# Optimization experiments

Measured on AMD Instinct MI355X. Metric: run time of the kernel, lower is better.

The kernel has to match this reference:

```python
import jax, jax.numpy as jnp
import numpy as np

HEADS = 8
EPS = 1e-5

def setup_inputs() -> dict:
    key = jax.random.key(0)
    k1, k2, k3 = jax.random.split(key, 3)
    b, c, n = 4, 512, 2048
    x = jax.random.normal(k1, (b, c, n), dtype=jnp.float32)
    g = jnp.ones((c,), dtype=jnp.float32)
    w_qkv = jax.random.normal(k2, (3 * c, c), dtype=jnp.float32) * (1.0 / np.sqrt(c))
    w_out = jax.random.normal(k3, (c, c), dtype=jnp.float32) * (1.0 / np.sqrt(c))
    b_out = jnp.zeros((c,), dtype=jnp.float32)
    return {"x": x, "g": g, "w_qkv": w_qkv, "w_out": w_out, "b_out": b_out}

def reference(x, g, w_qkv, w_out, b_out):
    b, c, n = x.shape
    h = HEADS
    d = c // h
    scale = d ** -0.5
    # channel LayerNorm (biased variance), scale g, no bias
    mean = jnp.mean(x, axis=1, keepdims=True)
    var = jnp.var(x, axis=1, keepdims=True)
    xn = (x - mean) * jax.lax.rsqrt(var + EPS) * g[None, :, None]
    # 1x1 conv == channel matmul: (3c, c) x (b, c, n) -> (b, 3c, n)
    qkv = jnp.einsum('oc,bcn->bon', w_qkv, xn)
    q, k, v = jnp.split(qkv, 3, axis=1)
    # b (h d) n -> b h d n
    q = q.reshape(b, h, d, n) * scale
    k = k.reshape(b, h, d, n)
    v = v.reshape(b, h, d, n)
    sim = jnp.einsum('bhdi,bhdj->bhij', q, k)  # [b,h,n,n]
    attn = jax.nn.softmax(sim, axis=-1)
    out = jnp.einsum('bhij,bhdj->bhid', attn, v)  # [b,h,n,d]
    out = out.transpose(0, 1, 3, 2).reshape(b, h * d, n)  # b (h d) n
    out = jnp.einsum('oc,bcn->bon', w_out, out) + b_out[None, :, None]
    return out
```

## Files before the change

### kernel.cpp

```cpp
#include <hip/hip_runtime.h>
#include <hip/hip_bf16.h>

#define B_ 4
#define C_ 512
#define N_ 2048
#define H_ 8
#define D_ 64
#define O3_ 1536
#define SPLIT 2
#define JTN 16

typedef __bf16 bf16x8 __attribute__((ext_vector_type(8)));
typedef float f32x4 __attribute__((ext_vector_type(4)));
typedef unsigned short ushort_t;

#define QSCALE 0.1803368801111137f

__device__ inline ushort_t f2b(float f) {
    __hip_bfloat16 h = __float2bfloat16(f);
    return *reinterpret_cast<ushort_t*>(&h);
}
__device__ inline float b2f(ushort_t u) {
    unsigned v = ((unsigned)u) << 16;
    return *reinterpret_cast<float*>(&v);
}

__device__ inline void gload16(const ushort_t* g, ushort_t* l) {
    __builtin_amdgcn_global_load_lds(
        (const __attribute__((address_space(1))) unsigned int*)g,
        (__attribute__((address_space(3))) unsigned int*)l, 16, 0, 0);
}

__global__ __launch_bounds__(256) void k_pre(const float* __restrict__ x,
                                             const float* __restrict__ g,
                                             ushort_t* __restrict__ xnT,
                                             const float* __restrict__ wqkv,
                                             const float* __restrict__ wout,
                                             ushort_t* __restrict__ wqkv_b,
                                             ushort_t* __restrict__ wout_b) {
    if (blockIdx.x >= 256) {
        int i = (blockIdx.x - 256) * 256 + threadIdx.x;
        float4 a = reinterpret_cast<const float4*>(wqkv)[i];
        ushort4 o;
        o.x = f2b(a.x); o.y = f2b(a.y); o.z = f2b(a.z); o.w = f2b(a.w);
        reinterpret_cast<ushort4*>(wqkv_b)[i] = o;
        if (i < 65536) {
            float4 c = reinterpret_cast<const float4*>(wout)[i];
            ushort4 oc;
            oc.x = f2b(c.x); oc.y = f2b(c.y); oc.z = f2b(c.z); oc.w = f2b(c.w);
            reinterpret_cast<ushort4*>(wout_b)[i] = oc;
        }
        return;
    }

    int bid = blockIdx.x;
    int b  = bid >> 6;
    int j0 = (bid & 63) * 32;
    int t  = threadIdx.x;

    __shared__ float s_red[8][32];
    __shared__ float s_red2[8][32];
    __shared__ float s_mean[32], s_rstd[32];
    __shared__ float s_g[C_];
    __shared__ __align__(16) ushort_t s_t[32][C_ + 2];

    for (int i = t; i < C_; i += 256) s_g[i] = g[i];

    int jl = t & 31, cg = t >> 5;
    const float* xb = x + (size_t)b * C_ * N_;

    float xv[64];
    float sum = 0.f, sq = 0.f;
#pragma unroll
    for (int i = 0; i < 64; ++i) {
        float v = xb[(size_t)(cg * 64 + i) * N_ + j0 + jl];
        xv[i] = v;
        sum += v; sq += v * v;
    }
    s_red[cg][jl] = sum; s_red2[cg][jl] = sq;
    __syncthreads();
    if (t < 32) {
        float s = 0.f, q = 0.f;
#pragma unroll
        for (int i = 0; i < 8; ++i) { s += s_red[i][t]; q += s_red2[i][t]; }
        float mean = s * (1.0f / C_);
        float var  = q * (1.0f / C_) - mean * mean;
        s_mean[t] = mean;
        s_rstd[t] = rsqrtf(var + 1e-5f);
    }
    __syncthreads();

    float mean = s_mean[jl], rstd = s_rstd[jl];
#pragma unroll
    for (int i = 0; i < 64; ++i) {
        int c = cg * 64 + i;
        s_t[jl][c] = f2b((xv[i] - mean) * rstd * s_g[c]);
    }
    __syncthreads();

    for (int jr = 0; jr < 32; ++jr) {
        unsigned val = *reinterpret_cast<const unsigned*>(&s_t[jr][t * 2]);
        *reinterpret_cast<unsigned*>(
            &xnT[((size_t)(b * N_ + j0 + jr)) * C_ + t * 2]) = val;
    }
}

template <int MODE>
__global__ __launch_bounds__(256) void k_gemm(const ushort_t* __restrict__ A,
                                              const ushort_t* __restrict__ Bt,
                                              ushort_t* __restrict__ qT,
                                              ushort_t* __restrict__ kT,
                                              ushort_t* __restrict__ vv,
                                              float* __restrict__ out,
                                              const float* __restrict__ b_out) {
    constexpr int M = (MODE == 0) ? O3_ : C_;
    constexpr int K = C_;
    constexpr int NMT = M / 128;
    constexpr int NWG = B_ * NMT * 16;

    int bid  = blockIdx.x;
    int sbid = (bid & 7) * (NWG / 8) + (bid >> 3);
    int b    = sbid / (NMT * 16);
    int rem  = sbid % (NMT * 16);
    int mt0  = (rem / 16) * 128;
    int nt0  = (rem % 16) * 128;

    int t = threadIdx.x;
    int w = t >> 6, lane = t & 63;
    int wm = (w >> 1) * 64, wn = (w & 1) * 64;
    int low = lane & 15, hi = lane >> 4;

    __shared__ __align__(16) ushort_t sA[128][64];
    __shared__ __align__(16) ushort_t sB[128][64];

    const ushort_t* Bb = Bt + (size_t)b * N_ * K;

    int srow = lane >> 3;
    int sseg = (lane & 7) ^ srow;
    const ushort_t* Ag = A  + (size_t)(mt0 + w * 32 + srow) * K + sseg * 8;
    const ushort_t* Bg = Bb + (size_t)(nt0 + w * 32 + srow) * K + sseg * 8;

    f32x4 acc[4][4] = {};

    for (int k0 = 0; k0 < K; k0 += 64) {
#pragma unroll
        for (int i = 0; i < 4; ++i) {
            gload16(Ag + (size_t)(i * 8) * K + k0, &sA[w * 32 + i * 8][0]);
            gload16(Bg + (size_t)(i * 8) * K + k0, &sB[w * 32 + i * 8][0]);
        }
        asm volatile("s_waitcnt vmcnt(0)" ::: "memory");
        __syncthreads();
#pragma unroll
        for (int kk = 0; kk < 64; kk += 32) {
            bf16x8 af[4], bfr[4];
#pragma unroll
            for (int mt = 0; mt < 4; ++mt) {
                int cseg = ((kk >> 3) + hi) ^ (low & 7);
                af[mt] = *reinterpret_cast<const bf16x8*>(
                    &sA[wm + mt * 16 + low][cseg * 8]);
            }
#pragma unroll
            for (int nt = 0; nt < 4; ++nt) {
                int cseg = ((kk >> 3) + hi) ^ (low & 7);
                bfr[nt] = *reinterpret_cast<const bf16x8*>(
                    &sB[wn + nt * 16 + low][cseg * 8]);
            }
#pragma unroll
            for (int mt = 0; mt < 4; ++mt)
#pragma unroll
                for (int nt = 0; nt < 4; ++nt)
                    acc[mt][nt] = __builtin_amdgcn_mfma_f32_16x16x32_bf16(
                        af[mt], bfr[nt], acc[mt][nt], 0, 0, 0);
        }
        __syncthreads();
    }

#pragma unroll
    for (int mt = 0; mt < 4; ++mt)
#pragma unroll
        for (int nt = 0; nt < 4; ++nt) {
            int m0 = mt0 + wm + mt * 16 + hi * 4;
            int j  = nt0 + wn + nt * 16 + low;
            if constexpr (MODE == 0) {
                if (m0 < 512) {
                    ushort4 pk;
                    pk.x = f2b(acc[mt][nt][0] * QSCALE);
                    pk.y = f2b(acc[mt][nt][1] * QSCALE);
                    pk.z = f2b(acc[mt][nt][2] * QSCALE);
                    pk.w = f2b(acc[mt][nt][3] * QSCALE);
                    *reinterpret_cast<ushort4*>(
                        &qT[(((size_t)(b * H_ + (m0 >> 6)) * N_) + j) * D_ +
                            (m0 & 63)]) = pk;
                } else if (m0 < 1024) {
                    int mm = m0 - 512;
                    ushort4 pk;
                    pk.x = f2b(acc[mt][nt][0]);
                    pk.y = f2b(acc[mt][nt][1]);
                    pk.z = f2b(acc[mt][nt][2]);
                    pk.w = f2b(acc[mt][nt][3]);
                    *reinterpret_cast<ushort4*>(
                        &kT[(((size_t)(b * H_ + (mm >> 6)) * N_) + j) * D_ +
                            (mm & 63)]) = pk;
                } else {
                    int mm0 = m0 - 1024;
#pragma unroll
                    for (int r = 0; r < 4; ++r)
                        vv[(((size_t)(b * H_ + (mm0 >> 6)) * D_) +
                            ((mm0 & 63) + r)) * N_ + j] = f2b(acc[mt][nt][r]);
                }
            } else {
#pragma unroll
                for (int r = 0; r < 4; ++r)
                    out[((size_t)(b * C_ + m0 + r)) * N_ + j] =
                        acc[mt][nt][r] + b_out[m0 + r];
            }
        }
}

__global__ __launch_bounds__(512, 4) void k_attn(const ushort_t* __restrict__ qT,
                                                 const ushort_t* __restrict__ kT,
                                                 const ushort_t* __restrict__ vv,
                                                 ushort_t* __restrict__ O0,
                                                 ushort_t* __restrict__ O1,
                                                 float* __restrict__ Lp) {
    int bid  = blockIdx.x;
    int sbid = ((bid & 7) << 6) | (bid >> 3);
    int it256 = sbid & 7;
    int s     = (sbid >> 3) & 1;
    int h     = (sbid >> 4) & 7;
    int b     = sbid >> 7;
    int i0    = it256 * 256;
    int t = threadIdx.x, w = t >> 6, lane = t & 63;
    int low = lane & 15, hi = lane >> 4;

    __shared__ ushort_t sK[2][64][64];
    __shared__ ushort_t sV[2][64][64];
    __shared__ __align__(16) ushort_t sPT[256][72];

    const ushort_t* qb = qT + ((size_t)(b * H_ + h)) * N_ * D_;
    const ushort_t* kb = kT + ((size_t)(b * H_ + h)) * N_ * D_;
    const ushort_t* vb = vv + ((size_t)(b * H_ + h)) * D_ * N_;

    int srow = lane >> 3;
    int sseg = (lane & 7) ^ srow;
    const ushort_t* kg = kb + (size_t)(w * 8 + srow) * D_ + sseg * 8;
    const ushort_t* vg = vb + (size_t)(w * 8 + srow) * N_ + sseg * 8;

    bf16x8 qf[2][2];
#pragma unroll
    for (int mt = 0; mt < 2; ++mt)
#pragma unroll
        for (int kx = 0; kx < 2; ++kx)
            qf[mt][kx] = *reinterpret_cast<const bf16x8*>(
                &qb[(size_t)(i0 + w * 32 + mt * 16 + low) * D_ + kx * 32 + hi * 8]);

    {
        int j0 = s * JTN * 64;
        gload16(kg + (size_t)j0 * D_, &sK[0][w * 8][0]);
        gload16(vg + j0,              &sV[0][w * 8][0]);
    }
    asm volatile("s_waitcnt vmcnt(0)" ::: "memory");
    __syncthreads();

    f32x4 oacc[2][4] = {};
    float lp0 = 0.f, lp1 = 0.f;
    int sw = (low & 7) * 8;

    int buf = 0;
    for (int jj = 0; jj < JTN; ++jj) {
        int j0c = (s * JTN + jj) * 64;

        if (jj + 1 < JTN) {
            int j0n = j0c + 64;
            gload16(kg + (size_t)j0n * D_, &sK[buf ^ 1][w * 8][0]);
            gload16(vg + j0n,              &sV[buf ^ 1][w * 8][0]);
        }

        f32x4 sacc[2][4] = {};
#pragma unroll
        for (int kx = 0; kx < 2; ++kx) {
            bf16x8 kfx[4];
#pragma unroll
            for (int nt = 0; nt < 4; ++nt)
                kfx[nt] = *reinterpret_cast<const bf16x8*>(
                    &sK[buf][nt * 16 + low][((kx * 4 + hi) * 8) ^ sw]);
#pragma unroll
            for (int mt = 0; mt < 2; ++mt)
#pragma unroll
                for (int nt = 0; nt < 4; ++nt)
                    sacc[mt][nt] = __builtin_amdgcn_mfma_f32_16x16x32_bf16(
                        kfx[nt], qf[mt][kx], sacc[mt][nt], 0, 0, 0);
        }

        bf16x8 vf[2][4];
#pragma unroll
        for (int kx = 0; kx < 2; ++kx)
#pragma unroll
            for (int dt = 0; dt < 4; ++dt)
                vf[kx][dt] = *reinterpret_cast<const bf16x8*>(
                    &sV[buf][dt * 16 + low][((kx * 4 + hi) * 8) ^ sw]);

#pragma unroll
        for (int mt = 0; mt < 2; ++mt) {
            int qrow = w * 32 + mt * 16 + low;
#pragma unroll
            for (int nt = 0; nt < 4; ++nt) {
                float p0 = __builtin_amdgcn_exp2f(sacc[mt][nt][0]);
                float p1 = __builtin_amdgcn_exp2f(sacc[mt][nt][1]);
                float p2 = __builtin_amdgcn_exp2f(sacc[mt][nt][2]);
                float p3 = __builtin_amdgcn_exp2f(sacc[mt][nt][3]);
                if (mt == 0) lp0 += (p0 + p1) + (p2 + p3);
                else         lp1 += (p0 + p1) + (p2 + p3);
                ushort4 pk;
                pk.x = f2b(p0); pk.y = f2b(p1); pk.z = f2b(p2); pk.w = f2b(p3);
                *reinterpret_cast<ushort4*>(&sPT[qrow][nt * 16 + hi * 4]) = pk;
            }
        }

#pragma unroll
        for (int kx = 0; kx < 2; ++kx) {
            bf16x8 ap0 = *reinterpret_cast<const bf16x8*>(
                &sPT[w * 32 + low][kx * 32 + hi * 8]);
            bf16x8 ap1 = *reinterpret_cast<const bf16x8*>(
                &sPT[w * 32 + 16 + low][kx * 32 + hi * 8]);
#pragma unroll
            for (int dt = 0; dt < 4; ++dt) {
                oacc[0][dt] = __builtin_amdgcn_mfma_f32_16x16x32_bf16(
                    ap0, vf[kx][dt], oacc[0][dt], 0, 0, 0);
                oacc[1][dt] = __builtin_amdgcn_mfma_f32_16x16x32_bf16(
                    ap1, vf[kx][dt], oacc[1][dt], 0, 0, 0);
            }
        }

        asm volatile("s_waitcnt vmcnt(0)" ::: "memory");
        __syncthreads();
        buf ^= 1;
    }

    lp0 += __shfl_xor(lp0, 16); lp0 += __shfl_xor(lp0, 32);
    lp1 += __shfl_xor(lp1, 16); lp1 += __shfl_xor(lp1, 32);

    float* lrow = Lp + ((size_t)((s * B_ + b) * H_ + h)) * N_ + i0 + w * 32;
    if (lane < 16) {
        lrow[low]      = lp0;
        lrow[16 + low] = lp1;
    }

    ushort_t* op = (s == 0 ? O0 : O1) +
                   ((size_t)(b * N_ + i0 + w * 32)) * C_ + h * D_;
#pragma unroll
    for (int mt = 0; mt < 2; ++mt)
#pragma unroll
        for (int dt = 0; dt < 4; ++dt)
#pragma unroll
            for (int r = 0; r < 4; ++r)
                op[(size_t)(mt * 16 + hi * 4 + r) * C_ + dt * 16 + low] =
                    f2b(oacc[mt][dt][r]);
}

__global__ __launch_bounds__(256) void k_comb(const ushort_t* __restrict__ O1,
                                              const float* __restrict__ Lp,
                                              ushort_t* __restrict__ attnT) {
    int tid = blockIdx.x * 256 + threadIdx.x;
    int d4 = (tid & 15) * 4;
    int i  = (tid >> 4) & (N_ - 1);
    int bh = tid >> 15;
    int b = bh >> 3, h = bh & 7;
    size_t idx = ((size_t)(b * N_ + i)) * C_ + h * D_ + d4;
    ushort4 a0 = *reinterpret_cast<const ushort4*>(&attnT[idx]);
    ushort4 a1 = *reinterpret_cast<const ushort4*>(&O1[idx]);
    float l = Lp[(size_t)bh * N_ + i] + Lp[(size_t)(B_ * H_ + bh) * N_ + i];
    float linv = 1.0f / l;
    ushort4 o;
    o.x = f2b((b2f(a0.x) + b2f(a1.x)) * linv);
    o.y = f2b((b2f(a0.y) + b2f(a1.y)) * linv);
    o.z = f2b((b2f(a0.z) + b2f(a1.z)) * linv);
    o.w = f2b((b2f(a0.w) + b2f(a1.w)) * linv);
    *reinterpret_cast<ushort4*>(&attnT[idx]) = o;
}

extern "C" void kernel_launch(void* const* d_in, const int* in_sizes, int n_in,
                              void* d_out, int out_size, void* d_ws, size_t ws_size,
                              hipStream_t stream) {
    const float* x    = (const float*)d_in[0];
    const float* g    = (const float*)d_in[1];
    const float* wqkv = (const float*)d_in[2];
    const float* wout = (const float*)d_in[3];
    const float* bout = (const float*)d_in[4];
    float* out = (float*)d_out;

    char* ws = (char*)d_ws;
    ushort_t* xnT    = (ushort_t*)(ws);
    ushort_t* qT     = (ushort_t*)(ws + (size_t)8  * 1024 * 1024);
    ushort_t* kT     = (ushort_t*)(ws + (size_t)16 * 1024 * 1024);
    ushort_t* vv     = (ushort_t*)(ws + (size_t)24 * 1024 * 1024);
    ushort_t* attnT  = (ushort_t*)(ws + (size_t)32 * 1024 * 1024);
    ushort_t* wqkv_b = (ushort_t*)(ws + (size_t)40 * 1024 * 1024);
    ushort_t* wout_b = (ushort_t*)(ws + (size_t)42 * 1024 * 1024);
    float*    Lp     = (float*)   (ws + (size_t)43 * 1024 * 1024);

    k_pre<<<dim3(1024), dim3(256), 0, stream>>>(
        x, g, xnT, wqkv, wout, wqkv_b, wout_b);
    k_gemm<0><<<dim3(B_ * (O3_ / 128) * (N_ / 128)), dim3(256), 0, stream>>>(
        wqkv_b, xnT, qT, kT, vv, nullptr, nullptr);
    k_attn<<<dim3(B_ * H_ * (N_ / 256) * SPLIT), dim3(512), 0, stream>>>(
        qT, kT, vv, attnT, xnT, Lp);
    k_comb<<<dim3(4096), dim3(256), 0, stream>>>(xnT, Lp, attnT);
    k_gemm<1><<<dim3(B_ * (C_ / 128) * (N_ / 128)), dim3(256), 0, stream>>>(
        wout_b, attnT, nullptr, nullptr, nullptr, out, bout);
}
```

Before: 92.67 us.

## Add four-way KV-split attention kernel with register permlane P transpose

Adds an alternative attention kernel that splits the key/value sequence four ways instead of two. It uses 256-thread blocks in which each wave covers 64 query rows, so each K/V tile loaded into shared memory is reused across more MFMAs. The softmax probabilities are packed to bf16 and rearranged into MFMA operand layout in registers with v_permlane32/16 swap instructions. A matching combine kernel sums four partial outputs and row sums. The new path is only taken when the workspace holds the extra partial buffers, and the extra split adds more partial-output write and reduction traffic.

```diff
diff --git a/kernel.cpp b/kernel.cpp
--- a/kernel.cpp
+++ b/kernel.cpp
@@ -23,6 +23,15 @@
 __device__ inline float b2f(ushort_t u) {
     unsigned v = ((unsigned)u) << 16;
     return *reinterpret_cast<float*>(&v);
+}
+__device__ inline unsigned pkbf(float a, float b) {
+    return (unsigned)f2b(a) | ((unsigned)f2b(b) << 16);
+}
+__device__ inline void pl32swap(unsigned& a, unsigned& b) {
+    asm volatile("v_permlane32_swap_b32 %0, %1" : "+v"(a), "+v"(b));
+}
+__device__ inline void pl16swap(unsigned& a, unsigned& b) {
+    asm volatile("v_permlane16_swap_b32 %0, %1" : "+v"(a), "+v"(b));
 }
 
 __device__ inline void gload16(const ushort_t* g, ushort_t* l) {
@@ -217,6 +226,154 @@
         }
 }
 
+__global__ __launch_bounds__(256, 2) void k_attn4(const ushort_t* __restrict__ qT,
+                                                  const ushort_t* __restrict__ kT,
+                                                  const ushort_t* __restrict__ vv,
+                                                  ushort_t* __restrict__ O0,
+                                                  ushort_t* __restrict__ O1,
+                                                  ushort_t* __restrict__ O2,
+                                                  ushort_t* __restrict__ O3,
+                                                  float* __restrict__ Lp) {
+    constexpr int JT4 = 8;
+    int bid  = blockIdx.x;
+    int sbid = (bid & 7) * 128 + (bid >> 3);
+    int it256 = sbid & 7;
+    int s     = (sbid >> 3) & 3;
+    int h     = (sbid >> 5) & 7;
+    int b     = sbid >> 8;
+    int i0    = it256 * 256;
+    int t = threadIdx.x, w = t >> 6, lane = t & 63;
+    int low = lane & 15, hi = lane >> 4;
+
+    __shared__ ushort_t sK[2][64][64];
+    __shared__ ushort_t sV[2][64][64];
+
+    const ushort_t* qb = qT + ((size_t)(b * H_ + h)) * N_ * D_;
+    const ushort_t* kb = kT + ((size_t)(b * H_ + h)) * N_ * D_;
+    const ushort_t* vb = vv + ((size_t)(b * H_ + h)) * D_ * N_;
+
+    int srow = lane >> 3;
+    int sseg = (lane & 7) ^ srow;
+    const ushort_t* kg = kb + (size_t)(w * 16 + srow) * D_ + sseg * 8;
+    const ushort_t* vg = vb + (size_t)(w * 16 + srow) * N_ + sseg * 8;
+
+    bf16x8 qf[4][2];
+#pragma unroll
+    for (int mt = 0; mt < 4; ++mt)
+#pragma unroll
+        for (int kx = 0; kx < 2; ++kx)
+            qf[mt][kx] = *reinterpret_cast<const bf16x8*>(
+                &qb[(size_t)(i0 + w * 64 + mt * 16 + low) * D_ + kx * 32 + hi * 8]);
+
+    {
+        int j0 = s * JT4 * 64;
+        gload16(kg + (size_t)j0 * D_,           &sK[0][w * 16][0]);
+        gload16(kg + (size_t)(j0 + 8) * D_,     &sK[0][w * 16 + 8][0]);
+        gload16(vg + j0,                        &sV[0][w * 16][0]);
+        gload16(vg + (size_t)8 * N_ + j0,       &sV[0][w * 16 + 8][0]);
+    }
+    asm volatile("s_waitcnt vmcnt(0)" ::: "memory");
+    __syncthreads();
+
+    f32x4 oacc[4][4] = {};
+    float lp[4] = {};
+    int sw = (low & 7) * 8;
+
+    int buf = 0;
+    for (int jj = 0; jj < JT4; ++jj) {
+        if (jj + 1 < JT4) {
+            int j0n = (s * JT4 + jj + 1) * 64;
+            gload16(kg + (size_t)j0n * D_,       &sK[buf ^ 1][w * 16][0]);
+            gload16(kg + (size_t)(j0n + 8) * D_, &sK[buf ^ 1][w * 16 + 8][0]);
+            gload16(vg + j0n,                    &sV[buf ^ 1][w * 16][0]);
+            gload16(vg + (size_t)8 * N_ + j0n,   &sV[buf ^ 1][w * 16 + 8][0]);
+        }
+
+        f32x4 sacc[4][4] = {};
+#pragma unroll
+        for (int kx = 0; kx < 2; ++kx) {
+            bf16x8 kfx[4];
+#pragma unroll
+            for (int nt = 0; nt < 4; ++nt)
+                kfx[nt] = *reinterpret_cast<const bf16x8*>(
+                    &sK[buf][nt * 16 + low][((kx * 4 + hi) * 8) ^ sw]);
+#pragma unroll
+            for (int mt = 0; mt < 4; ++mt)
+#pragma unroll
+                for (int nt = 0; nt < 4; ++nt)
+                    sacc[mt][nt] = __builtin_amdgcn_mfma_f32_16x16x32_bf16(
+                        kfx[nt], qf[mt][kx], sacc[mt][nt], 0, 0, 0);
+        }
+
+        bf16x8 vf[2][4];
+#pragma unroll
+        for (int kx = 0; kx < 2; ++kx)
+#pragma unroll
+            for (int dt = 0; dt < 4; ++dt)
+                vf[kx][dt] = *reinterpret_cast<const bf16x8*>(
+                    &sV[buf][dt * 16 + low][((kx * 4 + hi) * 8) ^ sw]);
+
+#pragma unroll
+        for (int mt = 0; mt < 4; ++mt) {
+            float p[4][4];
+#pragma unroll
+            for (int nt = 0; nt < 4; ++nt)
+#pragma unroll
+                for (int r = 0; r < 4; ++r) {
+                    p[nt][r] = __builtin_amdgcn_exp2f(sacc[mt][nt][r]);
+                    lp[mt] += p[nt][r];
+                }
+#pragma unroll
+            for (int kx = 0; kx < 2; ++kx) {
+                unsigned a0 = pkbf(p[2 * kx][0],     p[2 * kx][1]);
+                unsigned a1 = pkbf(p[2 * kx][2],     p[2 * kx][3]);
+                unsigned b0 = pkbf(p[2 * kx + 1][0], p[2 * kx + 1][1]);
+                unsigned b1 = pkbf(p[2 * kx + 1][2], p[2 * kx + 1][3]);
+                pl32swap(a0, b0);
+                pl16swap(a0, b0);
+                pl32swap(a1, b1);
+                pl16swap(a1, b1);
+                unsigned tw[4] = {a0, a1, b0, b1};
+                bf16x8 pb = *reinterpret_cast<const bf16x8*>(tw);
+#pragma unroll
+                for (int dt = 0; dt < 4; ++dt)
+                    oacc[mt][dt] = __builtin_amdgcn_mfma_f32_16x16x32_bf16(
+                        vf[kx][dt], pb, oacc[mt][dt], 0, 0, 0);
+            }
+        }
+
+        asm volatile("s_waitcnt vmcnt(0)" ::: "memory");
+        __syncthreads();
+        buf ^= 1;
+    }
+
+#pragma unroll
+    for (int mt = 0; mt < 4; ++mt) {
+        lp[mt] += __shfl_xor(lp[mt], 16);
+        lp[mt] += __shfl_xor(lp[mt], 32);
+    }
+    float* lrow = Lp + ((size_t)((s * B_ + b) * H_ + h)) * N_ + i0 + w * 64;
+    if (hi == 0) {
+#pragma unroll
+        for (int mt = 0; mt < 4; ++mt) lrow[mt * 16 + low] = lp[mt];
+    }
+
+    ushort_t* op = (s == 0 ? O0 : s == 1 ? O1 : s == 2 ? O2 : O3) +
+                   ((size_t)(b * N_ + i0 + w * 64)) * C_ + h * D_;
+#pragma unroll
+    for (int mt = 0; mt < 4; ++mt)
+#pragma unroll
+        for (int dt = 0; dt < 4; ++dt) {
+            ushort4 pk;
+            pk.x = f2b(oacc[mt][dt][0]);
+            pk.y = f2b(oacc[mt][dt][1]);
+            pk.z = f2b(oacc[mt][dt][2]);
+            pk.w = f2b(oacc[mt][dt][3]);
+            *reinterpret_cast<ushort4*>(
+                &op[(size_t)(mt * 16 + low) * C_ + dt * 16 + hi * 4]) = pk;
+        }
+}
+
 __global__ __launch_bounds__(512, 4) void k_attn(const ushort_t* __restrict__ qT,
                                                  const ushort_t* __restrict__ kT,
                                                  const ushort_t* __restrict__ vv,
@@ -269,7 +426,6 @@
     int buf = 0;
     for (int jj = 0; jj < JTN; ++jj) {
         int j0c = (s * JTN + jj) * 64;
-
         if (jj + 1 < JTN) {
             int j0n = j0c + 64;
             gload16(kg + (size_t)j0n * D_, &sK[buf ^ 1][w * 8][0]);
@@ -379,6 +535,36 @@
     *reinterpret_cast<ushort4*>(&attnT[idx]) = o;
 }
 
+__global__ __launch_bounds__(256) void k_comb4(const ushort_t* __restrict__ O1,
+                                               const ushort_t* __restrict__ O2,
+                                               const ushort_t* __restrict__ O3,
+                                               const float* __restrict__ Lp,
+                                               ushort_t* __restrict__ attnT) {
+    int tid = blockIdx.x * 256 + threadIdx.x;
+    int d4 = (tid & 15) * 4;
+    int i  = (tid >> 4) & (N_ - 1);
+    int bh = tid >> 15;
+    int b = bh >> 3, h = bh & 7;
+    size_t idx = ((size_t)(b * N_ + i)) * C_ + h * D_ + d4;
+
+    float l = 0.f;
+#pragma unroll
+    for (int s = 0; s < 4; ++s)
+        l += Lp[((size_t)(s * B_ * H_) + bh) * N_ + i];
+    float linv = 1.0f / l;
+
+    ushort4 a0 = *reinterpret_cast<const ushort4*>(&attnT[idx]);
+    ushort4 a1 = *reinterpret_cast<const ushort4*>(&O1[idx]);
+    ushort4 a2 = *reinterpret_cast<const ushort4*>(&O2[idx]);
+    ushort4 a3 = *reinterpret_cast<const ushort4*>(&O3[idx]);
+    ushort4 o;
+    o.x = f2b((b2f(a0.x) + b2f(a1.x) + b2f(a2.x) + b2f(a3.x)) * linv);
+    o.y = f2b((b2f(a0.y) + b2f(a1.y) + b2f(a2.y) + b2f(a3.y)) * linv);
+    o.z = f2b((b2f(a0.z) + b2f(a1.z) + b2f(a2.z) + b2f(a3.z)) * linv);
+    o.w = f2b((b2f(a0.w) + b2f(a1.w) + b2f(a2.w) + b2f(a3.w)) * linv);
+    *reinterpret_cast<ushort4*>(&attnT[idx]) = o;
+}
+
 extern "C" void kernel_launch(void* const* d_in, const int* in_sizes, int n_in,
                               void* d_out, int out_size, void* d_ws, size_t ws_size,
                               hipStream_t stream) {
@@ -398,14 +584,24 @@
     ushort_t* wqkv_b = (ushort_t*)(ws + (size_t)40 * 1024 * 1024);
     ushort_t* wout_b = (ushort_t*)(ws + (size_t)42 * 1024 * 1024);
     float*    Lp     = (float*)   (ws + (size_t)43 * 1024 * 1024);
+    ushort_t* O2     = (ushort_t*)(ws + (size_t)44 * 1024 * 1024);
+    ushort_t* O3     = (ushort_t*)(ws + (size_t)52 * 1024 * 1024);
+
+    bool sp4 = ws_size >= (size_t)60 * 1024 * 1024;
 
     k_pre<<<dim3(1024), dim3(256), 0, stream>>>(
         x, g, xnT, wqkv, wout, wqkv_b, wout_b);
     k_gemm<0><<<dim3(B_ * (O3_ / 128) * (N_ / 128)), dim3(256), 0, stream>>>(
         wqkv_b, xnT, qT, kT, vv, nullptr, nullptr);
-    k_attn<<<dim3(B_ * H_ * (N_ / 256) * SPLIT), dim3(512), 0, stream>>>(
-        qT, kT, vv, attnT, xnT, Lp);
-    k_comb<<<dim3(4096), dim3(256), 0, stream>>>(xnT, Lp, attnT);
+    if (sp4) {
+        k_attn4<<<dim3(1024), dim3(256), 0, stream>>>(
+            qT, kT, vv, attnT, xnT, O2, O3, Lp);
+        k_comb4<<<dim3(4096), dim3(256), 0, stream>>>(xnT, O2, O3, Lp, attnT);
+    } else {
+        k_attn<<<dim3(512), dim3(512), 0, stream>>>(
+            qT, kT, vv, attnT, xnT, Lp);
+        k_comb<<<dim3(4096), dim3(256), 0, stream>>>(xnT, Lp, attnT);
+    }
     k_gemm<1><<<dim3(B_ * (C_ / 128) * (N_ / 128)), dim3(256), 0, stream>>>(
         wout_b, attnT, nullptr, nullptr, nullptr, out, bout);
 }
```

Result: slower. 102.3 us (+10.4%).

## Keep softmax probabilities in registers via permlane swaps instead of LDS round-trip

Applied to the files above, without the earlier changes.

The P tile is no longer written to shared memory and read back as an MFMA operand. It is packed to bf16 and rearranged across lanes with v_permlane32_swap and v_permlane16_swap so it can feed the PV MFMA straight from registers. This drops the sPT buffer, cutting LDS traffic and LDS footprint. The launch-bounds occupancy hint also drops from 4 to 2, which gives the compiler more registers per thread but may lower waves per CU.

```diff
diff --git a/kernel.cpp b/kernel.cpp
--- a/kernel.cpp
+++ b/kernel.cpp
@@ -23,6 +23,15 @@
 __device__ inline float b2f(ushort_t u) {
     unsigned v = ((unsigned)u) << 16;
     return *reinterpret_cast<float*>(&v);
+}
+__device__ inline unsigned pkbf(float a, float b) {
+    return (unsigned)f2b(a) | ((unsigned)f2b(b) << 16);
+}
+__device__ inline void pl32swap(unsigned& a, unsigned& b) {
+    asm volatile("v_permlane32_swap_b32 %0, %1" : "+v"(a), "+v"(b));
+}
+__device__ inline void pl16swap(unsigned& a, unsigned& b) {
+    asm volatile("v_permlane16_swap_b32 %0, %1" : "+v"(a), "+v"(b));
 }
 
 __device__ inline void gload16(const ushort_t* g, ushort_t* l) {
@@ -217,7 +226,7 @@
         }
 }
 
-__global__ __launch_bounds__(512, 4) void k_attn(const ushort_t* __restrict__ qT,
+__global__ __launch_bounds__(512, 2) void k_attn(const ushort_t* __restrict__ qT,
                                                  const ushort_t* __restrict__ kT,
                                                  const ushort_t* __restrict__ vv,
                                                  ushort_t* __restrict__ O0,
@@ -235,7 +244,6 @@
 
     __shared__ ushort_t sK[2][64][64];
     __shared__ ushort_t sV[2][64][64];
-    __shared__ __align__(16) ushort_t sPT[256][72];
 
     const ushort_t* qb = qT + ((size_t)(b * H_ + h)) * N_ * D_;
     const ushort_t* kb = kT + ((size_t)(b * H_ + h)) * N_ * D_;
@@ -268,10 +276,8 @@
 
     int buf = 0;
     for (int jj = 0; jj < JTN; ++jj) {
-        int j0c = (s * JTN + jj) * 64;
-
         if (jj + 1 < JTN) {
-            int j0n = j0c + 64;
+            int j0n = (s * JTN + jj + 1) * 64;
             gload16(kg + (size_t)j0n * D_, &sK[buf ^ 1][w * 8][0]);
             gload16(vg + j0n,              &sV[buf ^ 1][w * 8][0]);
         }
@@ -302,33 +308,33 @@
 
 #pragma unroll
         for (int mt = 0; mt < 2; ++mt) {
-            int qrow = w * 32 + mt * 16 + low;
-#pragma unroll
-            for (int nt = 0; nt < 4; ++nt) {
-                float p0 = __builtin_amdgcn_exp2f(sacc[mt][nt][0]);
-                float p1 = __builtin_amdgcn_exp2f(sacc[mt][nt][1]);
-                float p2 = __builtin_amdgcn_exp2f(sacc[mt][nt][2]);
-                float p3 = __builtin_amdgcn_exp2f(sacc[mt][nt][3]);
-                if (mt == 0) lp0 += (p0 + p1) + (p2 + p3);
-                else         lp1 += (p0 + p1) + (p2 + p3);
-                ushort4 pk;
-                pk.x = f2b(p0); pk.y = f2b(p1); pk.z = f2b(p2); pk.w = f2b(p3);
-                *reinterpret_cast<ushort4*>(&sPT[qrow][nt * 16 + hi * 4]) = pk;
-            }
-        }
-
-#pragma unroll
-        for (int kx = 0; kx < 2; ++kx) {
-            bf16x8 ap0 = *reinterpret_cast<const bf16x8*>(
-                &sPT[w * 32 + low][kx * 32 + hi * 8]);
-            bf16x8 ap1 = *reinterpret_cast<const bf16x8*>(
-                &sPT[w * 32 + 16 + low][kx * 32 + hi * 8]);
-#pragma unroll
-            for (int dt = 0; dt < 4; ++dt) {
-                oacc[0][dt] = __builtin_amdgcn_mfma_f32_16x16x32_bf16(
-                    ap0, vf[kx][dt], oacc[0][dt], 0, 0, 0);
-                oacc[1][dt] = __builtin_amdgcn_mfma_f32_16x16x32_bf16(
-                    ap1, vf[kx][dt], oacc[1][dt], 0, 0, 0);
+            float p[4][4];
+#pragma unroll
+            for (int nt = 0; nt < 4; ++nt)
+#pragma unroll
+                for (int r = 0; r < 4; ++r)
+                    p[nt][r] = __builtin_amdgcn_exp2f(sacc[mt][nt][r]);
+            float ls = ((p[0][0] + p[0][1]) + (p[0][2] + p[0][3])) +
+                       ((p[1][0] + p[1][1]) + (p[1][2] + p[1][3])) +
+                       ((p[2][0] + p[2][1]) + (p[2][2] + p[2][3])) +
+                       ((p[3][0] + p[3][1]) + (p[3][2] + p[3][3]));
+            if (mt == 0) lp0 += ls; else lp1 += ls;
+#pragma unroll
+            for (int kx = 0; kx < 2; ++kx) {
+                unsigned a0 = pkbf(p[2 * kx][0],     p[2 * kx][1]);
+                unsigned a1 = pkbf(p[2 * kx][2],     p[2 * kx][3]);
+                unsigned b0 = pkbf(p[2 * kx + 1][0], p[2 * kx + 1][1]);
+                unsigned b1 = pkbf(p[2 * kx + 1][2], p[2 * kx + 1][3]);
+                pl32swap(a0, b0);
+                pl16swap(a0, b0);
+                pl32swap(a1, b1);
+                pl16swap(a1, b1);
+                unsigned tw[4] = {a0, a1, b0, b1};
+                bf16x8 pb = *reinterpret_cast<const bf16x8*>(tw);
+#pragma unroll
+                for (int dt = 0; dt < 4; ++dt)
+                    oacc[mt][dt] = __builtin_amdgcn_mfma_f32_16x16x32_bf16(
+                        pb, vf[kx][dt], oacc[mt][dt], 0, 0, 0);
             }
         }
 
```

New measurement: 102.6 us. +10.8%, slower.

## Fuse split-KV combine into output projection GEMM B-tile loading

Applied to the files above, without the earlier changes.

Drops the separate combine kernel. The output projection GEMM now reads both split-attention partial outputs and the two softmax denominators, normalizes them while loading, and writes the result as bf16 into LDS. The output GEMM tile also shrinks from 128x128 to 64x128, doubling its grid to 512 workgroups for better occupancy. This saves a kernel launch and a full read/write pass over the attention output, but each output-GEMM tile now re-reads O0/O1 once per M-tile using plain global loads rather than async LDS loads.

```diff
diff --git a/kernel.cpp b/kernel.cpp
--- a/kernel.cpp
+++ b/kernel.cpp
@@ -30,6 +30,7 @@
         (const __attribute__((address_space(1))) unsigned int*)g,
         (__attribute__((address_space(3))) unsigned int*)l, 16, 0, 0);
 }
+
 
 __global__ __launch_bounds__(256) void k_pre(const float* __restrict__ x,
                                              const float* __restrict__ g,
@@ -105,17 +106,13 @@
     }
 }
 
-template <int MODE>
-__global__ __launch_bounds__(256) void k_gemm(const ushort_t* __restrict__ A,
-                                              const ushort_t* __restrict__ Bt,
-                                              ushort_t* __restrict__ qT,
-                                              ushort_t* __restrict__ kT,
-                                              ushort_t* __restrict__ vv,
-                                              float* __restrict__ out,
-                                              const float* __restrict__ b_out) {
-    constexpr int M = (MODE == 0) ? O3_ : C_;
+__global__ __launch_bounds__(256) void k_gemm0(const ushort_t* __restrict__ A,
+                                               const ushort_t* __restrict__ Bt,
+                                               ushort_t* __restrict__ qT,
+                                               ushort_t* __restrict__ kT,
+                                               ushort_t* __restrict__ vv) {
     constexpr int K = C_;
-    constexpr int NMT = M / 128;
+    constexpr int NMT = O3_ / 128;
     constexpr int NWG = B_ * NMT * 16;
 
     int bid  = blockIdx.x;
@@ -181,38 +178,31 @@
         for (int nt = 0; nt < 4; ++nt) {
             int m0 = mt0 + wm + mt * 16 + hi * 4;
             int j  = nt0 + wn + nt * 16 + low;
-            if constexpr (MODE == 0) {
-                if (m0 < 512) {
-                    ushort4 pk;
-                    pk.x = f2b(acc[mt][nt][0] * QSCALE);
-                    pk.y = f2b(acc[mt][nt][1] * QSCALE);
-                    pk.z = f2b(acc[mt][nt][2] * QSCALE);
-                    pk.w = f2b(acc[mt][nt][3] * QSCALE);
-                    *reinterpret_cast<ushort4*>(
-                        &qT[(((size_t)(b * H_ + (m0 >> 6)) * N_) + j) * D_ +
-                            (m0 & 63)]) = pk;
-                } else if (m0 < 1024) {
-                    int mm = m0 - 512;
-                    ushort4 pk;
-                    pk.x = f2b(acc[mt][nt][0]);
-                    pk.y = f2b(acc[mt][nt][1]);
-                    pk.z = f2b(acc[mt][nt][2]);
-                    pk.w = f2b(acc[mt][nt][3]);
-                    *reinterpret_cast<ushort4*>(
-                        &kT[(((size_t)(b * H_ + (mm >> 6)) * N_) + j) * D_ +
-                            (mm & 63)]) = pk;
-                } else {
-                    int mm0 = m0 - 1024;
-#pragma unroll
-                    for (int r = 0; r < 4; ++r)
-                        vv[(((size_t)(b * H_ + (mm0 >> 6)) * D_) +
-                            ((mm0 & 63) + r)) * N_ + j] = f2b(acc[mt][nt][r]);
-                }
+            if (m0 < 512) {
+                ushort4 pk;
+                pk.x = f2b(acc[mt][nt][0] * QSCALE);
+                pk.y = f2b(acc[mt][nt][1] * QSCALE);
+                pk.z = f2b(acc[mt][nt][2] * QSCALE);
+                pk.w = f2b(acc[mt][nt][3] * QSCALE);
+                *reinterpret_cast<ushort4*>(
+                    &qT[(((size_t)(b * H_ + (m0 >> 6)) * N_) + j) * D_ +
+                        (m0 & 63)]) = pk;
+            } else if (m0 < 1024) {
+                int mm = m0 - 512;
+                ushort4 pk;
+                pk.x = f2b(acc[mt][nt][0]);
+                pk.y = f2b(acc[mt][nt][1]);
+                pk.z = f2b(acc[mt][nt][2]);
+                pk.w = f2b(acc[mt][nt][3]);
+                *reinterpret_cast<ushort4*>(
+                    &kT[(((size_t)(b * H_ + (mm >> 6)) * N_) + j) * D_ +
+                        (mm & 63)]) = pk;
             } else {
+                int mm0 = m0 - 1024;
 #pragma unroll
                 for (int r = 0; r < 4; ++r)
-                    out[((size_t)(b * C_ + m0 + r)) * N_ + j] =
-                        acc[mt][nt][r] + b_out[m0 + r];
+                    vv[(((size_t)(b * H_ + (mm0 >> 6)) * D_) +
+                        ((mm0 & 63) + r)) * N_ + j] = f2b(acc[mt][nt][r]);
             }
         }
 }
@@ -358,25 +348,107 @@
                     f2b(oacc[mt][dt][r]);
 }
 
-__global__ __launch_bounds__(256) void k_comb(const ushort_t* __restrict__ O1,
-                                              const float* __restrict__ Lp,
-                                              ushort_t* __restrict__ attnT) {
-    int tid = blockIdx.x * 256 + threadIdx.x;
-    int d4 = (tid & 15) * 4;
-    int i  = (tid >> 4) & (N_ - 1);
-    int bh = tid >> 15;
-    int b = bh >> 3, h = bh & 7;
-    size_t idx = ((size_t)(b * N_ + i)) * C_ + h * D_ + d4;
-    ushort4 a0 = *reinterpret_cast<const ushort4*>(&attnT[idx]);
-    ushort4 a1 = *reinterpret_cast<const ushort4*>(&O1[idx]);
-    float l = Lp[(size_t)bh * N_ + i] + Lp[(size_t)(B_ * H_ + bh) * N_ + i];
-    float linv = 1.0f / l;
-    ushort4 o;
-    o.x = f2b((b2f(a0.x) + b2f(a1.x)) * linv);
-    o.y = f2b((b2f(a0.y) + b2f(a1.y)) * linv);
-    o.z = f2b((b2f(a0.z) + b2f(a1.z)) * linv);
-    o.w = f2b((b2f(a0.w) + b2f(a1.w)) * linv);
-    *reinterpret_cast<ushort4*>(&attnT[idx]) = o;
+__global__ __launch_bounds__(256) void k_gemm1(const ushort_t* __restrict__ A,
+                                               const ushort_t* __restrict__ O0,
+                                               const ushort_t* __restrict__ O1,
+                                               const float* __restrict__ Lp,
+                                               float* __restrict__ out,
+                                               const float* __restrict__ b_out) {
+    constexpr int K = C_;
+    constexpr int NMT = C_ / 64;
+    constexpr int NWG = B_ * NMT * 16;
+
+    int bid  = blockIdx.x;
+    int sbid = (bid & 7) * (NWG / 8) + (bid >> 3);
+    int b    = sbid / (NMT * 16);
+    int rem  = sbid % (NMT * 16);
+    int mt0  = (rem / 16) * 64;
+    int nt0  = (rem % 16) * 128;
+
+    int t = threadIdx.x;
+    int w = t >> 6, lane = t & 63;
+    int wm = (w >> 1) * 32, wn = (w & 1) * 64;
+    int low = lane & 15, hi = lane >> 4;
+
+    __shared__ __align__(16) ushort_t sA[64][64];
+    __shared__ __align__(16) ushort_t sB[128][64];
+
+    int srow = lane >> 3;
+    int sseg = (lane & 7) ^ srow;
+    int wseg = lane & 7;
+    const ushort_t* Ag = A + (size_t)(mt0 + w * 16 + srow) * K + sseg * 8;
+
+    f32x4 acc[2][4] = {};
+
+    for (int k0 = 0; k0 < K; k0 += 64) {
+        int h = k0 >> 6;
+#pragma unroll
+        for (int i = 0; i < 2; ++i)
+            gload16(Ag + (size_t)(i * 8) * K + k0, &sA[w * 16 + i * 8][0]);
+
+#pragma unroll
+        for (int it = 0; it < 4; ++it) {
+            int jr = w * 32 + it * 8 + srow;
+            int j  = nt0 + jr;
+            size_t obase = ((size_t)(b * N_ + j)) * C_ + k0 + sseg * 8;
+            ushort4 a0 = *reinterpret_cast<const ushort4*>(&O0[obase]);
+            ushort4 a1 = *reinterpret_cast<const ushort4*>(&O0[obase + 4]);
+            ushort4 c0 = *reinterpret_cast<const ushort4*>(&O1[obase]);
+            ushort4 c1 = *reinterpret_cast<const ushort4*>(&O1[obase + 4]);
+            float l = Lp[((size_t)(b * H_ + h)) * N_ + j] +
+                      Lp[((size_t)((B_ + b) * H_ + h)) * N_ + j];
+            float linv = 1.0f / l;
+            ushort4 o0, o1;
+            o0.x = f2b((b2f(a0.x) + b2f(c0.x)) * linv);
+            o0.y = f2b((b2f(a0.y) + b2f(c0.y)) * linv);
+            o0.z = f2b((b2f(a0.z) + b2f(c0.z)) * linv);
+            o0.w = f2b((b2f(a0.w) + b2f(c0.w)) * linv);
+            o1.x = f2b((b2f(a1.x) + b2f(c1.x)) * linv);
+            o1.y = f2b((b2f(a1.y) + b2f(c1.y)) * linv);
+            o1.z = f2b((b2f(a1.z) + b2f(c1.z)) * linv);
+            o1.w = f2b((b2f(a1.w) + b2f(c1.w)) * linv);
+            *reinterpret_cast<ushort4*>(&sB[jr][wseg * 8])     = o0;
+            *reinterpret_cast<ushort4*>(&sB[jr][wseg * 8 + 4]) = o1;
+        }
+
+        asm volatile("s_waitcnt vmcnt(0)" ::: "memory");
+        __syncthreads();
+#pragma unroll
+        for (int kk = 0; kk < 64; kk += 32) {
+            bf16x8 af[2], bfr[4];
+#pragma unroll
+            for (int mt = 0; mt < 2; ++mt) {
+                int cseg = ((kk >> 3) + hi) ^ (low & 7);
+                af[mt] = *reinterpret_cast<const bf16x8*>(
+                    &sA[wm + mt * 16 + low][cseg * 8]);
+            }
+#pragma unroll
+            for (int nt = 0; nt < 4; ++nt) {
+                int cseg = ((kk >> 3) + hi) ^ (low & 7);
+                bfr[nt] = *reinterpret_cast<const bf16x8*>(
+                    &sB[wn + nt * 16 + low][cseg * 8]);
+            }
+#pragma unroll
+            for (int mt = 0; mt < 2; ++mt)
+#pragma unroll
+                for (int nt = 0; nt < 4; ++nt)
+                    acc[mt][nt] = __builtin_amdgcn_mfma_f32_16x16x32_bf16(
+                        af[mt], bfr[nt], acc[mt][nt], 0, 0, 0);
+        }
+        __syncthreads();
+    }
+
+#pragma unroll
+    for (int mt = 0; mt < 2; ++mt)
+#pragma unroll
+        for (int nt = 0; nt < 4; ++nt) {
+            int m0 = mt0 + wm + mt * 16 + hi * 4;
+            int j  = nt0 + wn + nt * 16 + low;
+#pragma unroll
+            for (int r = 0; r < 4; ++r)
+                out[((size_t)(b * C_ + m0 + r)) * N_ + j] =
+                    acc[mt][nt][r] + b_out[m0 + r];
+        }
 }
 
 extern "C" void kernel_launch(void* const* d_in, const int* in_sizes, int n_in,
@@ -394,18 +466,17 @@
     ushort_t* qT     = (ushort_t*)(ws + (size_t)8  * 1024 * 1024);
     ushort_t* kT     = (ushort_t*)(ws + (size_t)16 * 1024 * 1024);
     ushort_t* vv     = (ushort_t*)(ws + (size_t)24 * 1024 * 1024);
-    ushort_t* attnT  = (ushort_t*)(ws + (size_t)32 * 1024 * 1024);
+    ushort_t* O0     = (ushort_t*)(ws + (size_t)32 * 1024 * 1024);
     ushort_t* wqkv_b = (ushort_t*)(ws + (size_t)40 * 1024 * 1024);
     ushort_t* wout_b = (ushort_t*)(ws + (size_t)42 * 1024 * 1024);
     float*    Lp     = (float*)   (ws + (size_t)43 * 1024 * 1024);
 
     k_pre<<<dim3(1024), dim3(256), 0, stream>>>(
         x, g, xnT, wqkv, wout, wqkv_b, wout_b);
-    k_gemm<0><<<dim3(B_ * (O3_ / 128) * (N_ / 128)), dim3(256), 0, stream>>>(
-        wqkv_b, xnT, qT, kT, vv, nullptr, nullptr);
+    k_gemm0<<<dim3(B_ * (O3_ / 128) * (N_ / 128)), dim3(256), 0, stream>>>(
+        wqkv_b, xnT, qT, kT, vv);
     k_attn<<<dim3(B_ * H_ * (N_ / 256) * SPLIT), dim3(512), 0, stream>>>(
-        qT, kT, vv, attnT, xnT, Lp);
-    k_comb<<<dim3(4096), dim3(256), 0, stream>>>(xnT, Lp, attnT);
-    k_gemm<1><<<dim3(B_ * (C_ / 128) * (N_ / 128)), dim3(256), 0, stream>>>(
-        wout_b, attnT, nullptr, nullptr, nullptr, out, bout);
-}
+        qT, kT, vv, O0, xnT, Lp);
+    k_gemm1<<<dim3(B_ * (C_ / 64) * (N_ / 128)), dim3(256), 0, stream>>>(
+        wout_b, O0, xnT, Lp, out, bout);
+}
```

New measurement: 92.87 us (median of 2 runs). Within noise of the previous version (+0.2%).
